# Kernel tuning notes

Measured on AMD Instinct MI355X. Metric: run time of the kernel, lower is better.

Reference implementation:

```python
import jax, jax.numpy as jnp
import numpy as np

B, N, D, K, H, HID, ITERS = 16, 4096, 64, 8, 4, 256, 3
DH = D // H
EPS = 1e-5


def _ln(x, g, b):
    m = x.mean(-1, keepdims=True)
    v = x.var(-1, keepdims=True)
    return (x - m) / jnp.sqrt(v + EPS) * g + b


def setup_inputs() -> dict:
    ks = jax.random.split(jax.random.key(0), 16)
    s = 1.0 / np.sqrt(D)
    return {
        "embeddings": jax.random.normal(ks[0], (B, N, D), dtype=jnp.float32),
        "slots_mu": jax.random.normal(ks[1], (1, K, D), dtype=jnp.float32) * 0.1,
        "slots_logsigma": jax.random.normal(ks[2], (1, K, D), dtype=jnp.float32) * 0.1,
        "mixing_init": jnp.full((1, K), 1.0 / K, dtype=jnp.float32),
        "to_keys": jax.random.uniform(ks[3], (K, D, D), dtype=jnp.float32),
        "to_queries": jax.random.uniform(ks[4], (K, D, D), dtype=jnp.float32),
        "to_values": jax.random.uniform(ks[5], (K, D, D), dtype=jnp.float32),
        "w_ih": jax.random.uniform(ks[6], (3 * D, D), minval=-s, maxval=s),
        "w_hh": jax.random.uniform(ks[7], (3 * D, D), minval=-s, maxval=s),
        "b_ih": jax.random.uniform(ks[8], (3 * D,), minval=-s, maxval=s),
        "b_hh": jax.random.uniform(ks[9], (3 * D,), minval=-s, maxval=s),
        "w1": jax.random.uniform(ks[10], (HID, D), minval=-s, maxval=s),
        "b1": jnp.zeros((HID,), jnp.float32),
        "w2": jax.random.uniform(ks[11], (D, HID), minval=-1.0 / np.sqrt(HID), maxval=1.0 / np.sqrt(HID)),
        "b2": jnp.zeros((D,), jnp.float32),
        "ln_in_g": jnp.ones((D,), jnp.float32), "ln_in_b": jnp.zeros((D,), jnp.float32),
        "ln_sl_g": jnp.ones((D,), jnp.float32), "ln_sl_b": jnp.zeros((D,), jnp.float32),
        "ln_ff_g": jnp.ones((D,), jnp.float32), "ln_ff_b": jnp.zeros((D,), jnp.float32),
        "noise_init": jax.random.normal(ks[12], (B, K, D), dtype=jnp.float32),
        "noise_final": jax.random.normal(ks[13], (B, K, D), dtype=jnp.float32),
    }


def reference(embeddings, slots_mu, slots_logsigma, mixing_init, to_keys, to_queries,
              to_values, w_ih, w_hh, b_ih, b_hh, w1, b1, w2, b2,
              ln_in_g, ln_in_b, ln_sl_g, ln_sl_b, ln_ff_g, ln_ff_b,
              noise_init, noise_final):
    mu = jnp.broadcast_to(slots_mu, (B, K, D))
    sigma = jnp.broadcast_to(jnp.exp(slots_logsigma), (B, K, D))
    slots = mu + sigma * noise_init                              # [B,K,D]
    mixing = jnp.broadcast_to(mixing_init, (B, K))[:, :, None]   # [B,K,1]

    x = _ln(embeddings, ln_in_g, ln_in_b)                        # [B,N,D]
    keys = jnp.einsum('bne,ked->bknd', x, to_keys).reshape(B, K, N, H, DH)
    values = jnp.einsum('bne,ked->bknd', x, to_values).reshape(B, K, N, H, DH)
    sigma = sigma.reshape(B, K, H, DH)
    # torch.einsum('bkd,kdd->bkd') uses the DIAGONAL of to_queries
    qdiag = jnp.einsum('kdd->kd', to_queries)                    # [K,D]
    log_pi = -0.5 * D * np.log(2.0 * np.pi)

    attn_vis = None
    for _ in range(ITERS):
        slots_prev = slots
        s_ln = _ln(slots, ln_sl_g, ln_sl_b)
        queries = (s_ln * qdiag[None]).reshape(B, K, H, DH)      # [B,K,H,Dh]
        exponent = -0.5 * (keys - queries[:, :, None]) ** 2 / (sigma[:, :, None] ** 2 + EPS)
        log_scale = -jnp.log(jnp.clip(sigma, EPS, None))[:, :, None]  # [B,K,1,H,Dh]
        gll = jnp.log(mixing + EPS)[..., None] + (log_pi + log_scale + exponent).sum(-1)  # [B,K,N,H]
        attn = jax.nn.softmax(gll, axis=1) + EPS
        attn_vis = attn
        Nk = attn.sum(axis=(2, 3))[:, :, None]                   # [B,K,1]
        upd = jnp.einsum('bknh,bknhd->bkhd', attn, values).reshape(B, K, D)
        upd = (1.0 / Nk + EPS) * upd
        nq = upd.reshape(B, K, H, DH)                            # source overwrites new_queries with slot_updates
        sig2 = jnp.einsum('bknh,bknhd->bkhd', attn, (keys - nq[:, :, None]) ** 2).reshape(B, K, D)
        sigma = (jnp.sqrt(sig2 / Nk) + EPS).reshape(B, K, H, DH)
        mixing = Nk / N
        # GRUCell (torch gate order: reset, update, new)
        xg = upd.reshape(-1, D) @ w_ih.T + b_ih
        hg = slots_prev.reshape(-1, D) @ w_hh.T + b_hh
        xr, xz, xn = jnp.split(xg, 3, axis=-1)
        hr, hz, hn = jnp.split(hg, 3, axis=-1)
        r = jax.nn.sigmoid(xr + hr)
        z = jax.nn.sigmoid(xz + hz)
        n = jnp.tanh(xn + r * hn)
        slots = ((1.0 - z) * n + z * slots_prev.reshape(-1, D)).reshape(B, K, D)
        pre = _ln(slots, ln_ff_g, ln_ff_b)
        slots = slots + jax.nn.relu(pre @ w1.T + b1) @ w2.T + b2

    sigma = sigma.reshape(B, K, D)
    slots = slots + sigma * noise_final
    return slots, attn_vis
```

## Files before the change

kernel.cpp:

```cpp
#include <hip/hip_runtime.h>
#include <math.h>

#define B_ 16
#define N_ 4096
#define D_ 64
#define K_ 8
#define H_ 4
#define HID_ 256
#define ITERS_ 3
#define EPS_ 1e-5f

#define PREC_ 3104

#define HTERM_ (-940.9930580015849f)

__device__ __forceinline__ float waveReduceSum64(float v) {
  v += __shfl_xor(v, 1);  v += __shfl_xor(v, 2);  v += __shfl_xor(v, 4);
  v += __shfl_xor(v, 8);  v += __shfl_xor(v, 16); v += __shfl_xor(v, 32);
  return v;
}
__device__ __forceinline__ float groupReduceSum16(float v) {
  v += __shfl_xor(v, 1); v += __shfl_xor(v, 2); v += __shfl_xor(v, 4);
  v += __shfl_xor(v, 8);
  return v;
}

template <int CTRL>
__device__ __forceinline__ float dpp_mov(float v) {
  return __int_as_float(__builtin_amdgcn_update_dpp(
      0, __float_as_int(v), CTRL, 0xF, 0xF, true));
}
__device__ __forceinline__ float row16Sum(float v) {
  v += dpp_mov<0xB1>(v);
  v += dpp_mov<0x4E>(v);
  v += dpp_mov<0x124>(v);
  v += dpp_mov<0x128>(v);
  return v;
}

__global__ void ln_emb_kernel(const float* __restrict__ emb,
                              const float* __restrict__ g, const float* __restrict__ b,
                              float* __restrict__ x, int b0) {
  int wave = threadIdx.x >> 6, lane = threadIdx.x & 63;
  int row = blockIdx.x * 4 + wave;
  float e = emb[((size_t)b0 * N_ + row) * 64 + lane];
  float s  = waveReduceSum64(e);
  float sq = waveReduceSum64(e * e);
  float mean = s * (1.0f / 64.0f);
  float var  = sq * (1.0f / 64.0f) - mean * mean;
  float inv  = rsqrtf(var + EPS_);
  x[(size_t)row * 64 + lane] = (e - mean) * inv * g[lane] + b[lane];
}

__global__ __launch_bounds__(256) void key_kernel(const float* __restrict__ x,
    const float* __restrict__ Wk, float* __restrict__ keys) {
  __shared__ float xs[64 * 65];
  __shared__ float wks[64 * 64];
  int n0 = blockIdx.x * 64;
  int k  = blockIdx.y;
  int bl = blockIdx.z;
  int tid = threadIdx.x;

  const float* xb = x + ((size_t)bl * N_ + n0) * 64;
  for (int i = tid; i < 4096; i += 256)
    xs[(i >> 6) * 65 + (i & 63)] = xb[i];
  const float4* wk4 = (const float4*)(Wk + (size_t)k * 4096);
  float4* wks4 = (float4*)wks;
  for (int i = tid; i < 1024; i += 256) wks4[i] = wk4[i];
  __syncthreads();

  int tr = tid >> 4, tc = tid & 15;
  int r0 = tr * 4, c0 = tc * 4;
  float ak[4][4] = {{0.f}};
  #pragma unroll 4
  for (int kk = 0; kk < 64; ++kk) {
    float xv[4];
    #pragma unroll
    for (int i = 0; i < 4; ++i) xv[i] = xs[(r0 + i) * 65 + kk];
    float4 wkq = *(const float4*)&wks[kk * 64 + c0];
    float wkc[4] = {wkq.x, wkq.y, wkq.z, wkq.w};
    #pragma unroll
    for (int i = 0; i < 4; ++i)
      #pragma unroll
      for (int j = 0; j < 4; ++j)
        ak[i][j] = fmaf(xv[i], wkc[j], ak[i][j]);
  }
  size_t outb = ((size_t)bl * N_ + n0) * 512 + (size_t)k * 64;
  #pragma unroll
  for (int i = 0; i < 4; ++i) {
    float4 kq = make_float4(ak[i][0], ak[i][1], ak[i][2], ak[i][3]);
    *(float4*)&keys[outb + (size_t)(r0 + i) * 512 + c0] = kq;
  }
}

__global__ void init_kernel(const float* __restrict__ mu, const float* __restrict__ lsig,
                            const float* __restrict__ mix0, const float* __restrict__ noise,
                            const float* __restrict__ tq,
                            const float* __restrict__ g_sl, const float* __restrict__ b_sl,
                            float* __restrict__ slots, float* __restrict__ q,
                            float* __restrict__ i2s, float* __restrict__ base, int b0) {
  int bk = b0 * K_ + blockIdx.x;
  int lane = threadIdx.x;
  int k = bk & (K_ - 1);
  int kd = k * 64 + lane;
  float sg = expf(lsig[kd]);
  float s = mu[kd] + sg * noise[bk * 64 + lane];
  slots[bk * 64 + lane] = s;
  float su = waveReduceSum64(s);
  float sq = waveReduceSum64(s * s);
  float mean = su * (1.0f / 64.0f);
  float var  = sq * (1.0f / 64.0f) - mean * mean;
  float sl = (s - mean) * rsqrtf(var + EPS_) * g_sl[lane] + b_sl[lane];
  q[bk * 64 + lane] = sl * tq[k * 4096 + lane * 65];
  i2s[bk * 64 + lane] = 0.5f / (sg * sg + EPS_);
  float ls = -logf(fmaxf(sg, EPS_));
  float lss = groupReduceSum16(ls);
  if ((lane & 15) == 0)
    base[bk * 4 + (lane >> 4)] = logf(mix0[k] + EPS_) + HTERM_ + lss;
}

template <bool WRITE_ATTN>
__global__ __launch_bounds__(256, 4) void attn_kernel(
    const float* __restrict__ keys, const float* __restrict__ x,
    const float* __restrict__ q, const float* __restrict__ i2s, const float* __restrict__ base,
    float* __restrict__ P, float* __restrict__ attn_out, int b0) {
  int bl = blockIdx.y;
  int bg = b0 + bl;
  int wave = threadIdx.x >> 6, lane = threadIdx.x & 63;
  int h = lane >> 4;
  int n0 = (blockIdx.x * 4 + wave) * 16;

  __shared__ float att_lds[4][K_][64];
  __shared__ float blk[PREC_];
  __shared__ float bv_lds[32];
  for (int i = threadIdx.x; i < PREC_; i += 256) blk[i] = 0.0f;
  if (threadIdx.x < 32) bv_lds[threadIdx.x] = base[bg * 32 + threadIdx.x];

  float qv[K_], iv[K_];
  {
    const float* qp = q + bg * 512 + lane;
    const float* ip = i2s + bg * 512 + lane;
    #pragma unroll
    for (int k = 0; k < K_; ++k) { qv[k] = qp[k * 64]; iv[k] = ip[k * 64]; }
  }
  float s1a[K_] = {0.f}, s2a[K_] = {0.f};
  __syncthreads();

  const float* kptr = keys + ((size_t)bl * N_ + n0) * 512 + lane;
  #pragma unroll 2
  for (int ni = 0; ni < 16; ++ni) {
    float key[K_], gl[K_];
    #pragma unroll
    for (int k = 0; k < K_; ++k) key[k] = kptr[k * 64];
    #pragma unroll
    for (int k = 0; k < K_; ++k) {
      float df = key[k] - qv[k];
      float t = row16Sum(df * df * iv[k]);
      gl[k] = bv_lds[k * 4 + h] - t;
    }
    float m = gl[0];
    #pragma unroll
    for (int k = 1; k < K_; ++k) m = fmaxf(m, gl[k]);
    float ssum = 0.f;
    #pragma unroll
    for (int k = 0; k < K_; ++k) { gl[k] = __expf(gl[k] - m); ssum += gl[k]; }
    float inv = __builtin_amdgcn_rcpf(ssum);
    #pragma unroll
    for (int k = 0; k < K_; ++k) {
      float a = gl[k] * inv + EPS_;
      s1a[k] = fmaf(a, key[k], s1a[k]);
      s2a[k] = fmaf(a * key[k], key[k], s2a[k]);
      if ((lane & 15) == 0) att_lds[wave][k][ni * 4 + h] = a;
    }
    kptr += 512;
  }
  #pragma unroll
  for (int k = 0; k < K_; ++k) {
    atomicAdd(&blk[k * 64 + lane],       s1a[k]);
    atomicAdd(&blk[512 + k * 64 + lane], s2a[k]);
  }

  float xr[16];
  {
    const float* xptr = x + ((size_t)bl * N_ + n0) * 64 + lane;
    #pragma unroll
    for (int ni = 0; ni < 16; ++ni) xr[ni] = xptr[ni * 64];
  }
  #pragma unroll
  for (int k = 0; k < K_; ++k) {
    float t0 = 0.f, t1 = 0.f, t2 = 0.f, t3 = 0.f;
    float c0 = 0.f, c1 = 0.f, c2 = 0.f, c3 = 0.f;
    #pragma unroll
    for (int ni = 0; ni < 16; ++ni) {
      float4 a4 = *(const float4*)&att_lds[wave][k][ni * 4];
      float xv = xr[ni];
      t0 = fmaf(a4.x, xv, t0); t1 = fmaf(a4.y, xv, t1);
      t2 = fmaf(a4.z, xv, t2); t3 = fmaf(a4.w, xv, t3);
      c0 += a4.x; c1 += a4.y; c2 += a4.z; c3 += a4.w;
    }
    atomicAdd(&blk[1024 + k * 256 + lane],       t0);
    atomicAdd(&blk[1024 + k * 256 + 64 + lane],  t1);
    atomicAdd(&blk[1024 + k * 256 + 128 + lane], t2);
    atomicAdd(&blk[1024 + k * 256 + 192 + lane], t3);
    if (lane == 0) {
      atomicAdd(&blk[3072 + k * 4 + 0], c0);
      atomicAdd(&blk[3072 + k * 4 + 1], c1);
      atomicAdd(&blk[3072 + k * 4 + 2], c2);
      atomicAdd(&blk[3072 + k * 4 + 3], c3);
    }
  }
  __syncthreads();
  {
    float4* p4 = (float4*)(P + ((size_t)bl * 64 + blockIdx.x) * PREC_);
    const float4* b4 = (const float4*)blk;
    for (int i = threadIdx.x; i < PREC_ / 4; i += 256) p4[i] = b4[i];
  }
  if (WRITE_ATTN) {
    #pragma unroll
    for (int k = 0; k < K_; ++k)
      attn_out[((size_t)(bg * K_ + k) * N_ + n0) * 4 + lane] = att_lds[wave][k][lane];
  }
}

__global__ __launch_bounds__(256) void update_kernel(
    const float* __restrict__ P, const float* __restrict__ Wv,
    float* __restrict__ slots,
    const float* __restrict__ w_ih, const float* __restrict__ w_hh,
    const float* __restrict__ b_ih, const float* __restrict__ b_hh,
    const float* __restrict__ w1, const float* __restrict__ b1,
    const float* __restrict__ w2, const float* __restrict__ b2,
    const float* __restrict__ g_ff, const float* __restrict__ b_ff,
    const float* __restrict__ tq,
    const float* __restrict__ g_sl, const float* __restrict__ b_sl,
    float* __restrict__ q, float* __restrict__ i2s, float* __restrict__ base,
    const float* __restrict__ noise_final, float* __restrict__ out_slots,
    int last, int b0) {
  int bx = blockIdx.x;
  int bl = bx >> 3;
  int bk = b0 * K_ + bx;
  int k = bx & (K_ - 1);
  int t = threadIdx.x;
  __shared__ float S1_s[64], S2_s[64], T_s[256], S0_s[4];
  __shared__ float upd_s[64], sp_s[64], sig_s[64], xg_s[192], hg_s[192],
                   snew_s[64], pre_s[64], hid_s[256];

  {
    int off0;
    if (t < 64)        off0 = k * 64 + t;
    else if (t < 128)  off0 = 512 + k * 64 + (t - 64);
    else               off0 = 1024 + k * 256 + (t - 128);
    int j1 = t + 256;
    int off1 = -1;
    if (j1 < 384)      off1 = 1024 + k * 256 + (j1 - 128);
    else if (j1 < 388) off1 = 3072 + k * 4 + (j1 - 384);
    float acc0 = 0.f, acc1 = 0.f;
    const float* Pb = P + (size_t)bl * 64 * PREC_;
    #pragma unroll 4
    for (int a = 0; a < 64; ++a) {
      const float* pa = Pb + (size_t)a * PREC_;
      acc0 += pa[off0];
      if (off1 >= 0) acc1 += pa[off1];
    }
    if (t < 64)       S1_s[t] = acc0;
    else if (t < 128) S2_s[t - 64] = acc0;
    else              T_s[t - 128] = acc0;
    if (t < 128)      T_s[t + 128] = acc1;
    else if (t < 132) S0_s[t - 128] = acc1;
  }
  __syncthreads();

  if (t < 64) {
    float nk = S0_s[0] + S0_s[1] + S0_s[2] + S0_s[3];
    float sv = 0.f;
    const float* Trow = &T_s[(t >> 4) * 64];
    const float* wv = Wv + (size_t)k * 4096 + t;
    #pragma unroll 8
    for (int e = 0; e < 64; ++e) sv = fmaf(Trow[e], wv[(size_t)e * 64], sv);
    float upd = (1.0f / nk + EPS_) * sv;
    upd_s[t] = upd;
    float s1 = S1_s[t], s2 = S2_s[t], s0 = S0_s[t >> 4];
    float sig2 = fmaxf(s2 - 2.0f * upd * s1 + upd * upd * s0, 0.0f);
    sig_s[t] = sqrtf(sig2 / nk) + EPS_;
    sp_s[t] = slots[bk * 64 + t];
  }
  __syncthreads();
  if (t < 192) {
    const float4* wr = (const float4*)(w_ih + t * 64);
    const float4* wh = (const float4*)(w_hh + t * 64);
    float a1 = b_ih[t], a2 = b_hh[t];
    #pragma unroll
    for (int d4 = 0; d4 < 16; ++d4) {
      float4 wa = wr[d4], wb = wh[d4];
      const float* u  = &upd_s[d4 * 4];
      const float* sp = &sp_s[d4 * 4];
      a1 += u[0] * wa.x + u[1] * wa.y + u[2] * wa.z + u[3] * wa.w;
      a2 += sp[0] * wb.x + sp[1] * wb.y + sp[2] * wb.z + sp[3] * wb.w;
    }
    xg_s[t] = a1;
    hg_s[t] = a2;
  }
  __syncthreads();
  if (t < 64) {
    float r = 1.0f / (1.0f + expf(-(xg_s[t] + hg_s[t])));
    float z = 1.0f / (1.0f + expf(-(xg_s[64 + t] + hg_s[64 + t])));
    float nn = tanhf(xg_s[128 + t] + r * hg_s[128 + t]);
    float sn = (1.0f - z) * nn + z * sp_s[t];
    snew_s[t] = sn;
    float su = waveReduceSum64(sn);
    float sq = waveReduceSum64(sn * sn);
    float mean = su * (1.0f / 64.0f);
    float var  = sq * (1.0f / 64.0f) - mean * mean;
    pre_s[t] = (sn - mean) * rsqrtf(var + EPS_) * g_ff[t] + b_ff[t];
  }
  __syncthreads();
  {
    const float4* w1r = (const float4*)(w1 + t * 64);
    float a = b1[t];
    #pragma unroll
    for (int d4 = 0; d4 < 16; ++d4) {
      float4 w = w1r[d4];
      const float* p = &pre_s[d4 * 4];
      a += p[0] * w.x + p[1] * w.y + p[2] * w.z + p[3] * w.w;
    }
    hid_s[t] = fmaxf(a, 0.0f);
  }
  __syncthreads();
  if (t < 64) {
    const float4* w2r = (const float4*)(w2 + t * 256);
    float a = b2[t];
    #pragma unroll
    for (int j4 = 0; j4 < 64; ++j4) {
      float4 w = w2r[j4];
      const float* p = &hid_s[j4 * 4];
      a += p[0] * w.x + p[1] * w.y + p[2] * w.z + p[3] * w.w;
    }
    float outv = snew_s[t] + a;
    slots[bk * 64 + t] = outv;
    if (last) {
      out_slots[bk * 64 + t] = outv + sig_s[t] * noise_final[bk * 64 + t];
    } else {
      float su = waveReduceSum64(outv);
      float sq = waveReduceSum64(outv * outv);
      float mean = su * (1.0f / 64.0f);
      float var  = sq * (1.0f / 64.0f) - mean * mean;
      float sl = (outv - mean) * rsqrtf(var + EPS_) * g_sl[t] + b_sl[t];
      q[bk * 64 + t] = sl * tq[k * 4096 + t * 65];
      float sg = sig_s[t];
      i2s[bk * 64 + t] = 0.5f / (sg * sg + EPS_);
      float ls = -logf(fmaxf(sg, EPS_));
      float lss = groupReduceSum16(ls);
      float nk = S0_s[0] + S0_s[1] + S0_s[2] + S0_s[3];
      if ((t & 15) == 0)
        base[bk * 4 + (t >> 4)] = logf(nk * (1.0f / (float)N_) + EPS_) + HTERM_ + lss;
    }
  }
}

extern "C" void kernel_launch(void* const* d_in, const int* in_sizes, int n_in,
                              void* d_out, int out_size, void* d_ws, size_t ws_size,
                              hipStream_t stream) {
  const float* emb  = (const float*)d_in[0];
  const float* mu   = (const float*)d_in[1];
  const float* lsig = (const float*)d_in[2];
  const float* mix0 = (const float*)d_in[3];
  const float* Wk   = (const float*)d_in[4];
  const float* Wq   = (const float*)d_in[5];
  const float* Wv   = (const float*)d_in[6];
  const float* w_ih = (const float*)d_in[7];
  const float* w_hh = (const float*)d_in[8];
  const float* b_ih = (const float*)d_in[9];
  const float* b_hh = (const float*)d_in[10];
  const float* w1   = (const float*)d_in[11];
  const float* b1   = (const float*)d_in[12];
  const float* w2   = (const float*)d_in[13];
  const float* b2   = (const float*)d_in[14];
  const float* g_in = (const float*)d_in[15];
  const float* b_in = (const float*)d_in[16];
  const float* g_sl = (const float*)d_in[17];
  const float* b_sl = (const float*)d_in[18];
  const float* g_ff = (const float*)d_in[19];
  const float* b_ff = (const float*)d_in[20];
  const float* nz0  = (const float*)d_in[21];
  const float* nzf  = (const float*)d_in[22];

  float* ws = (float*)d_ws;
  float* slots = ws;
  float* q     = slots + 8192;
  float* i2s   = q + 8192;
  float* base  = i2s + 8192;
  float* x     = base + 512;
  const size_t small_bytes = (size_t)(3 * 8192 + 512) * 4;
  const size_t per_batch = (size_t)(N_ * 64 + N_ * 512 + 64 * PREC_) * 4;

  int C = 16;
  while (C > 1 && small_bytes + (size_t)C * per_batch > ws_size) C >>= 1;
  float* keys = x + (size_t)C * N_ * 64;
  float* P    = keys + (size_t)C * N_ * 512;

  float* out_slots = (float*)d_out;
  float* out_attn  = out_slots + B_ * K_ * 64;

  for (int b0 = 0; b0 < B_; b0 += C) {
    ln_emb_kernel<<<dim3(C * N_ / 4), 256, 0, stream>>>(emb, g_in, b_in, x, b0);
    key_kernel<<<dim3(N_ / 64, K_, C), 256, 0, stream>>>(x, Wk, keys);
    init_kernel<<<dim3(C * K_), 64, 0, stream>>>(mu, lsig, mix0, nz0, Wq, g_sl, b_sl,
                                                 slots, q, i2s, base, b0);
    for (int it = 0; it < ITERS_; ++it) {
      int last = (it == ITERS_ - 1) ? 1 : 0;
      if (last)
        attn_kernel<true><<<dim3(N_ / 64, C), 256, 0, stream>>>(keys, x, q, i2s, base,
                                                                P, out_attn, b0);
      else
        attn_kernel<false><<<dim3(N_ / 64, C), 256, 0, stream>>>(keys, x, q, i2s, base,
                                                                 P, nullptr, b0);
      update_kernel<<<dim3(C * K_), 256, 0, stream>>>(P, Wv, slots,
          w_ih, w_hh, b_ih, b_hh, w1, b1, w2, b2, g_ff, b_ff,
          Wq, g_sl, b_sl, q, i2s, base, nzf, out_slots, last, b0);
    }
  }
}
```

Before: 540.0 us.

## Reuse x tile across slots in key kernel; widen attention blocks to 512 threads

The key projection kernel now loads each 64-row x tile once, stored transposed so rows can be read as float4, and loops over all K slot weight matrices instead of launching one block per slot. This removes repeated x loads and the strided LDS reads, at the cost of fewer blocks and an extra barrier per slot. The attention kernel uses 512-thread blocks with 8 waves, each handling 8 rows instead of 16. This is meant to raise wave parallelism and shorten per-wave serial work. The x row loads are also issued before the LDS atomics so their latency overlaps.

```diff
diff --git a/kernel.cpp b/kernel.cpp
--- a/kernel.cpp
+++ b/kernel.cpp
@@ -54,42 +54,48 @@
 
 __global__ __launch_bounds__(256) void key_kernel(const float* __restrict__ x,
     const float* __restrict__ Wk, float* __restrict__ keys) {
-  __shared__ float xs[64 * 65];
+  __shared__ float xst[64 * 68];
   __shared__ float wks[64 * 64];
   int n0 = blockIdx.x * 64;
-  int k  = blockIdx.y;
-  int bl = blockIdx.z;
+  int bl = blockIdx.y;
   int tid = threadIdx.x;
 
   const float* xb = x + ((size_t)bl * N_ + n0) * 64;
-  for (int i = tid; i < 4096; i += 256)
-    xs[(i >> 6) * 65 + (i & 63)] = xb[i];
-  const float4* wk4 = (const float4*)(Wk + (size_t)k * 4096);
-  float4* wks4 = (float4*)wks;
-  for (int i = tid; i < 1024; i += 256) wks4[i] = wk4[i];
-  __syncthreads();
+  for (int i = tid; i < 4096; i += 256) {
+    int n = i >> 6, e = i & 63;
+    xst[e * 68 + n] = xb[i];
+  }
 
   int tr = tid >> 4, tc = tid & 15;
   int r0 = tr * 4, c0 = tc * 4;
-  float ak[4][4] = {{0.f}};
-  #pragma unroll 4
-  for (int kk = 0; kk < 64; ++kk) {
-    float xv[4];
-    #pragma unroll
-    for (int i = 0; i < 4; ++i) xv[i] = xs[(r0 + i) * 65 + kk];
-    float4 wkq = *(const float4*)&wks[kk * 64 + c0];
-    float wkc[4] = {wkq.x, wkq.y, wkq.z, wkq.w};
-    #pragma unroll
-    for (int i = 0; i < 4; ++i)
+  size_t outb = ((size_t)bl * N_ + n0) * 512;
+
+  for (int k = 0; k < K_; ++k) {
+    __syncthreads();
+    const float4* wk4 = (const float4*)(Wk + (size_t)k * 4096);
+    float4* wks4 = (float4*)wks;
+    for (int i = tid; i < 1024; i += 256) wks4[i] = wk4[i];
+    __syncthreads();
+
+    float ak[4][4] = {{0.f}};
+    #pragma unroll 8
+    for (int kk = 0; kk < 64; ++kk) {
+      float4 xq = *(const float4*)&xst[kk * 68 + r0];
+      float4 wq = *(const float4*)&wks[kk * 64 + c0];
+      float xv[4] = {xq.x, xq.y, xq.z, xq.w};
+      float wc[4] = {wq.x, wq.y, wq.z, wq.w};
       #pragma unroll
-      for (int j = 0; j < 4; ++j)
-        ak[i][j] = fmaf(xv[i], wkc[j], ak[i][j]);
-  }
-  size_t outb = ((size_t)bl * N_ + n0) * 512 + (size_t)k * 64;
-  #pragma unroll
-  for (int i = 0; i < 4; ++i) {
-    float4 kq = make_float4(ak[i][0], ak[i][1], ak[i][2], ak[i][3]);
-    *(float4*)&keys[outb + (size_t)(r0 + i) * 512 + c0] = kq;
+      for (int i = 0; i < 4; ++i)
+        #pragma unroll
+        for (int j = 0; j < 4; ++j)
+          ak[i][j] = fmaf(xv[i], wc[j], ak[i][j]);
+    }
+    size_t ob = outb + (size_t)k * 64;
+    #pragma unroll
+    for (int i = 0; i < 4; ++i) {
+      float4 kq = make_float4(ak[i][0], ak[i][1], ak[i][2], ak[i][3]);
+      *(float4*)&keys[ob + (size_t)(r0 + i) * 512 + c0] = kq;
+    }
   }
 }
 
@@ -120,7 +126,7 @@
 }
 
 template <bool WRITE_ATTN>
-__global__ __launch_bounds__(256, 4) void attn_kernel(
+__global__ __launch_bounds__(512, 8) void attn_kernel(
     const float* __restrict__ keys, const float* __restrict__ x,
     const float* __restrict__ q, const float* __restrict__ i2s, const float* __restrict__ base,
     float* __restrict__ P, float* __restrict__ attn_out, int b0) {
@@ -128,12 +134,12 @@
   int bg = b0 + bl;
   int wave = threadIdx.x >> 6, lane = threadIdx.x & 63;
   int h = lane >> 4;
-  int n0 = (blockIdx.x * 4 + wave) * 16;
-
-  __shared__ float att_lds[4][K_][64];
+  int n0 = blockIdx.x * 64 + wave * 8;
+
+  __shared__ float att_lds[8][K_][32];
   __shared__ float blk[PREC_];
   __shared__ float bv_lds[32];
-  for (int i = threadIdx.x; i < PREC_; i += 256) blk[i] = 0.0f;
+  for (int i = threadIdx.x; i < PREC_; i += 512) blk[i] = 0.0f;
   if (threadIdx.x < 32) bv_lds[threadIdx.x] = base[bg * 32 + threadIdx.x];
 
   float qv[K_], iv[K_];
@@ -147,8 +153,8 @@
   __syncthreads();
 
   const float* kptr = keys + ((size_t)bl * N_ + n0) * 512 + lane;
-  #pragma unroll 2
-  for (int ni = 0; ni < 16; ++ni) {
+  #pragma unroll
+  for (int ni = 0; ni < 8; ++ni) {
     float key[K_], gl[K_];
     #pragma unroll
     for (int k = 0; k < K_; ++k) key[k] = kptr[k * 64];
@@ -174,24 +180,25 @@
     }
     kptr += 512;
   }
+
+  float xr[8];
+  {
+    const float* xptr = x + ((size_t)bl * N_ + n0) * 64 + lane;
+    #pragma unroll
+    for (int ni = 0; ni < 8; ++ni) xr[ni] = xptr[ni * 64];
+  }
   #pragma unroll
   for (int k = 0; k < K_; ++k) {
     atomicAdd(&blk[k * 64 + lane],       s1a[k]);
     atomicAdd(&blk[512 + k * 64 + lane], s2a[k]);
   }
 
-  float xr[16];
-  {
-    const float* xptr = x + ((size_t)bl * N_ + n0) * 64 + lane;
-    #pragma unroll
-    for (int ni = 0; ni < 16; ++ni) xr[ni] = xptr[ni * 64];
-  }
   #pragma unroll
   for (int k = 0; k < K_; ++k) {
     float t0 = 0.f, t1 = 0.f, t2 = 0.f, t3 = 0.f;
     float c0 = 0.f, c1 = 0.f, c2 = 0.f, c3 = 0.f;
     #pragma unroll
-    for (int ni = 0; ni < 16; ++ni) {
+    for (int ni = 0; ni < 8; ++ni) {
       float4 a4 = *(const float4*)&att_lds[wave][k][ni * 4];
       float xv = xr[ni];
       t0 = fmaf(a4.x, xv, t0); t1 = fmaf(a4.y, xv, t1);
@@ -213,12 +220,14 @@
   {
     float4* p4 = (float4*)(P + ((size_t)bl * 64 + blockIdx.x) * PREC_);
     const float4* b4 = (const float4*)blk;
-    for (int i = threadIdx.x; i < PREC_ / 4; i += 256) p4[i] = b4[i];
+    for (int i = threadIdx.x; i < PREC_ / 4; i += 512) p4[i] = b4[i];
   }
   if (WRITE_ATTN) {
-    #pragma unroll
-    for (int k = 0; k < K_; ++k)
-      attn_out[((size_t)(bg * K_ + k) * N_ + n0) * 4 + lane] = att_lds[wave][k][lane];
+    if (lane < 32) {
+      #pragma unroll
+      for (int k = 0; k < K_; ++k)
+        attn_out[((size_t)(bg * K_ + k) * N_ + n0) * 4 + lane] = att_lds[wave][k][lane];
+    }
   }
 }
 
@@ -402,16 +411,16 @@
 
   for (int b0 = 0; b0 < B_; b0 += C) {
     ln_emb_kernel<<<dim3(C * N_ / 4), 256, 0, stream>>>(emb, g_in, b_in, x, b0);
-    key_kernel<<<dim3(N_ / 64, K_, C), 256, 0, stream>>>(x, Wk, keys);
+    key_kernel<<<dim3(N_ / 64, C), 256, 0, stream>>>(x, Wk, keys);
     init_kernel<<<dim3(C * K_), 64, 0, stream>>>(mu, lsig, mix0, nz0, Wq, g_sl, b_sl,
                                                  slots, q, i2s, base, b0);
     for (int it = 0; it < ITERS_; ++it) {
       int last = (it == ITERS_ - 1) ? 1 : 0;
       if (last)
-        attn_kernel<true><<<dim3(N_ / 64, C), 256, 0, stream>>>(keys, x, q, i2s, base,
+        attn_kernel<true><<<dim3(N_ / 64, C), 512, 0, stream>>>(keys, x, q, i2s, base,
                                                                 P, out_attn, b0);
       else
-        attn_kernel<false><<<dim3(N_ / 64, C), 256, 0, stream>>>(keys, x, q, i2s, base,
+        attn_kernel<false><<<dim3(N_ / 64, C), 512, 0, stream>>>(keys, x, q, i2s, base,
                                                                  P, nullptr, b0);
       update_kernel<<<dim3(C * K_), 256, 0, stream>>>(P, Wv, slots,
           w_ih, w_hh, b_ih, b_hh, w1, b1, w2, b2, g_ff, b_ff,
```

Result: slower. 952.3 us (+76.3%).
